# Optimization experiments

Measured on AMD Instinct MI355X. Metric: run time of the kernel, lower is better.

## Reference

```python
import jax, jax.numpy as jnp
import numpy as np

UP = 2
CUTOFF = 1.0 / UP  # factor = 1


def make_recon_rect(N, cutoff):
    """Reconstruction low-pass rect for rfft2, shape [N, N//2+1]."""
    lo = int(N * cutoff // 2)
    hi = int(N - lo)
    r = np.ones(N, dtype=np.float32)
    r[lo + 1:hi] = 0.0
    if N % 4 == 0:
        r[lo] = 0.5
        r[hi] = 0.5
    rect2d = r[:, None] * r[None, :]          # [N, N]
    return jnp.asarray(rect2d[:, :N // 2 + 1])  # keep rfft half-spectrum


def setup_inputs() -> dict:
    key = jax.random.key(0)
    x = jax.random.normal(key, (16, 64, 128, 128), dtype=jnp.float32)
    return {"x": x}


def reference(x):
    B, C, H, W = x.shape
    Hu, Wu = H * UP, W * UP
    # zero-insertion upsample: sample at (i*UP, j*UP), zeros elsewhere
    z = jnp.zeros((B, C, Hu, Wu), dtype=x.dtype).at[:, :, ::UP, ::UP].set(x)
    rect = make_recon_rect(Wu, CUTOFF)         # [Wu, Wu//2+1]
    xf = jnp.fft.rfft2(z) * rect               # low-pass in frequency domain
    out = jnp.fft.irfft2(xf) * (UP ** 2)       # gain correction
    return out
```

## Files before the change

kernel.cpp:

```cpp
#include <hip/hip_runtime.h>


typedef __bf16 bf16x8 __attribute__((ext_vector_type(8)));
typedef float  f32x4  __attribute__((ext_vector_type(4)));

#define W2 136
#define PI_F 3.14159265358979323846f

__device__ __forceinline__ unsigned short f2bf(float x) {
    unsigned int b = __float_as_uint(x);
    return (unsigned short)((b + 0x7FFFu + ((b >> 16) & 1u)) >> 16);
}

__device__ __forceinline__ float gfun(int j) {
    int d = 2 * (j & 127) + 1;
    float th = PI_F * (float)d * (1.0f / 256.0f);
    float s  = ((d & 3) == 1) ? 1.0f : -1.0f;
    return s * cosf(th) / (128.0f * sinf(th));
}

__global__ __launch_bounds__(512)
void init_ghtab(unsigned short* __restrict__ ghtab)
{
    const int t   = threadIdx.x;
    const int lane = t & 63;
    const int l15 = lane & 15;
    const int l4  = lane >> 4;
    const int dd  = t >> 6;
    const int base = l15 - 8 * l4 + 16 * dd;
    unsigned short u[8];
    #pragma unroll
    for (int e = 0; e < 8; ++e) u[e] = f2bf(gfun(base - e));
    ushort4 a = make_ushort4(u[0], u[1], u[2], u[3]);
    ushort4 b = make_ushort4(u[4], u[5], u[6], u[7]);
    *(ushort4*)&ghtab[t * 8]     = a;
    *(ushort4*)&ghtab[t * 8 + 4] = b;
}

__global__ __launch_bounds__(512, 4)
void upsample_fused(const float* __restrict__ xin, float* __restrict__ out,
                    const unsigned short* __restrict__ ghtab)
{
    __shared__ __align__(16) unsigned short Et[256 * W2];
    __shared__ float gtab[128];

    const int tid  = threadIdx.x;
    const int lane = tid & 63;
    const int w    = tid >> 6;
    const int l15  = lane & 15;
    const int l4   = lane >> 4;

    const float* __restrict__ xim = xin + (long long)blockIdx.x * (128 * 128);
    float*       __restrict__ oim = out + (long long)blockIdx.x * (256 * 256);

    const int r = 16 * w + l15;
    const float* __restrict__ xrow = xim + r * 128;

    float4 xlo[4], xhi[4];
    #pragma unroll
    for (int t = 0; t < 4; ++t) {
        xlo[t] = *(const float4*)&xrow[32 * t + 8 * l4];
        xhi[t] = *(const float4*)&xrow[32 * t + 8 * l4 + 4];
    }

    bf16x8 gh[8];
    if (ghtab) {
        #pragma unroll
        for (int dd = 0; dd < 8; ++dd)
            gh[dd] = *(const bf16x8*)&ghtab[(dd * 64 + lane) * 8];
    } else {
        if (tid < 128) gtab[tid] = gfun(tid);
        __syncthreads();
        #pragma unroll
        for (int dd = 0; dd < 8; ++dd) {
            union { bf16x8 v; unsigned short u[8]; } H;
            int base = l15 - 8 * l4 + 16 * dd;
            #pragma unroll
            for (int e = 0; e < 8; ++e) H.u[e] = f2bf(gtab[(base - e) & 127]);
            gh[dd] = H.v;
        }
    }

    bf16x8 xa[4];
    #pragma unroll
    for (int t = 0; t < 4; ++t) {
        union { bf16x8 v; unsigned short u[8]; } H;
        H.u[0] = f2bf(xlo[t].x); H.u[1] = f2bf(xlo[t].y);
        H.u[2] = f2bf(xlo[t].z); H.u[3] = f2bf(xlo[t].w);
        H.u[4] = f2bf(xhi[t].x); H.u[5] = f2bf(xhi[t].y);
        H.u[6] = f2bf(xhi[t].z); H.u[7] = f2bf(xhi[t].w);
        xa[t] = H.v;
        const int m0 = 32 * t + 8 * l4;
        #pragma unroll
        for (int e = 0; e < 8; ++e)
            Et[(2 * (m0 + e)) * W2 + r] = H.u[e];
    }

    float* __restrict__ orow = oim + (2 * r) * 256;
    #pragma unroll
    for (int mt = 0; mt < 8; ++mt) {
        f32x4 acc = {0.f, 0.f, 0.f, 0.f};
        #pragma unroll
        for (int t = 0; t < 4; ++t)
            acc = __builtin_amdgcn_mfma_f32_16x16x32_bf16(gh[(mt - 2 * t) & 7], xa[t], acc, 0, 0, 0);
        const int i0 = 16 * mt + 4 * l4;
        float4 xc = *(const float4*)&xrow[i0];
        float4 o0 = make_float4(xc.x, acc[0], xc.y, acc[1]);
        float4 o1 = make_float4(xc.z, acc[2], xc.w, acc[3]);
        *(float4*)&orow[2 * i0]     = o0;
        *(float4*)&orow[2 * i0 + 4] = o1;
        #pragma unroll
        for (int q = 0; q < 4; ++q)
            Et[(2 * (i0 + q) + 1) * W2 + r] = f2bf(acc[q]);
    }
    __syncthreads();

    {
        float* __restrict__ prow = oim + (2 * (16 * w + l15) + 1) * 256;
        #pragma unroll
        for (int mc = 0; mc < 16; ++mc) {
            f32x4 acc = {0.f, 0.f, 0.f, 0.f};
            #pragma unroll
            for (int t = 0; t < 4; ++t) {
                bf16x8 ef = *(const bf16x8*)&Et[(16 * mc + l15) * W2 + 32 * t + 8 * l4];
                acc = __builtin_amdgcn_mfma_f32_16x16x32_bf16(ef, gh[(w - 2 * t) & 7], acc, 0, 0, 0);
            }
            float4 o = make_float4(acc[0], acc[1], acc[2], acc[3]);
            *(float4*)&prow[16 * mc + 4 * l4] = o;
        }
    }
}

extern "C" void kernel_launch(void* const* d_in, const int* in_sizes, int n_in,
                              void* d_out, int out_size, void* d_ws, size_t ws_size,
                              hipStream_t stream)
{
    (void)n_in; (void)out_size;
    const float* x = (const float*)d_in[0];
    float* out = (float*)d_out;
    int nimg = in_sizes[0] / (128 * 128);

    unsigned short* ghtab = nullptr;
    if (ws_size >= 8192) {
        ghtab = (unsigned short*)d_ws;
        hipLaunchKernelGGL(init_ghtab, dim3(1), dim3(512), 0, stream, ghtab);
    }
    hipLaunchKernelGGL(upsample_fused, dim3(nimg), dim3(512), 0, stream, x, out, ghtab);
}
```

Before: 105.9 us.

## Split each image across two blocks by output column half, halving LDS

Each image is now handled by two blocks, each computing one half of the output columns. The split halves the shared-memory transpose buffer and raises the occupancy hint from 4 to 8 blocks per CU. Each block still loads the full input image and builds the full coefficient table, so that work is duplicated across the pair. Conversions now use native __bf16 casts instead of the manual rounding helper.

```diff
diff --git a/kernel.cpp b/kernel.cpp
--- a/kernel.cpp
+++ b/kernel.cpp
@@ -22,26 +22,24 @@
 __global__ __launch_bounds__(512)
 void init_ghtab(unsigned short* __restrict__ ghtab)
 {
-    const int t   = threadIdx.x;
+    const int t    = threadIdx.x;
     const int lane = t & 63;
-    const int l15 = lane & 15;
-    const int l4  = lane >> 4;
-    const int dd  = t >> 6;
+    const int l15  = lane & 15;
+    const int l4   = lane >> 4;
+    const int dd   = t >> 6;
     const int base = l15 - 8 * l4 + 16 * dd;
     unsigned short u[8];
     #pragma unroll
     for (int e = 0; e < 8; ++e) u[e] = f2bf(gfun(base - e));
-    ushort4 a = make_ushort4(u[0], u[1], u[2], u[3]);
-    ushort4 b = make_ushort4(u[4], u[5], u[6], u[7]);
-    *(ushort4*)&ghtab[t * 8]     = a;
-    *(ushort4*)&ghtab[t * 8 + 4] = b;
+    *(ushort4*)&ghtab[t * 8]     = make_ushort4(u[0], u[1], u[2], u[3]);
+    *(ushort4*)&ghtab[t * 8 + 4] = make_ushort4(u[4], u[5], u[6], u[7]);
 }
 
-__global__ __launch_bounds__(512, 4)
+__global__ __launch_bounds__(512, 8)
 void upsample_fused(const float* __restrict__ xin, float* __restrict__ out,
                     const unsigned short* __restrict__ ghtab)
 {
-    __shared__ __align__(16) unsigned short Et[256 * W2];
+    __shared__ __align__(16) __bf16 Et[128 * W2];
     __shared__ float gtab[128];
 
     const int tid  = threadIdx.x;
@@ -50,8 +48,10 @@
     const int l15  = lane & 15;
     const int l4   = lane >> 4;
 
-    const float* __restrict__ xim = xin + (long long)blockIdx.x * (128 * 128);
-    float*       __restrict__ oim = out + (long long)blockIdx.x * (256 * 256);
+    const long long img = blockIdx.x >> 1;
+    const int cb        = blockIdx.x & 1;
+    const float* __restrict__ xim = xin + img * (128LL * 128LL);
+    float*       __restrict__ oim = out + img * (256LL * 256LL);
 
     const int r = 16 * w + l15;
     const float* __restrict__ xrow = xim + r * 128;
@@ -81,49 +81,52 @@
         }
     }
 
-    bf16x8 xa[4];
+    union { bf16x8 v; __bf16 h[8]; } xa[4];
     #pragma unroll
     for (int t = 0; t < 4; ++t) {
-        union { bf16x8 v; unsigned short u[8]; } H;
-        H.u[0] = f2bf(xlo[t].x); H.u[1] = f2bf(xlo[t].y);
-        H.u[2] = f2bf(xlo[t].z); H.u[3] = f2bf(xlo[t].w);
-        H.u[4] = f2bf(xhi[t].x); H.u[5] = f2bf(xhi[t].y);
-        H.u[6] = f2bf(xhi[t].z); H.u[7] = f2bf(xhi[t].w);
-        xa[t] = H.v;
-        const int m0 = 32 * t + 8 * l4;
+        xa[t].h[0] = (__bf16)xlo[t].x; xa[t].h[1] = (__bf16)xlo[t].y;
+        xa[t].h[2] = (__bf16)xlo[t].z; xa[t].h[3] = (__bf16)xlo[t].w;
+        xa[t].h[4] = (__bf16)xhi[t].x; xa[t].h[5] = (__bf16)xhi[t].y;
+        xa[t].h[6] = (__bf16)xhi[t].z; xa[t].h[7] = (__bf16)xhi[t].w;
+    }
+    #pragma unroll
+    for (int tt = 0; tt < 2; ++tt) {
+        const int t = 2 * cb + tt;
         #pragma unroll
         for (int e = 0; e < 8; ++e)
-            Et[(2 * (m0 + e)) * W2 + r] = H.u[e];
+            Et[(64 * tt + 16 * l4 + 2 * e) * W2 + r] = xa[t].h[e];
     }
 
-    float* __restrict__ orow = oim + (2 * r) * 256;
+    float* __restrict__ orow = oim + (2 * r) * 256 + 128 * cb;
     #pragma unroll
-    for (int mt = 0; mt < 8; ++mt) {
+    for (int mt = 0; mt < 4; ++mt) {
         f32x4 acc = {0.f, 0.f, 0.f, 0.f};
         #pragma unroll
         for (int t = 0; t < 4; ++t)
-            acc = __builtin_amdgcn_mfma_f32_16x16x32_bf16(gh[(mt - 2 * t) & 7], xa[t], acc, 0, 0, 0);
-        const int i0 = 16 * mt + 4 * l4;
-        float4 xc = *(const float4*)&xrow[i0];
+            acc = __builtin_amdgcn_mfma_f32_16x16x32_bf16(gh[(4 * cb + mt - 2 * t) & 7],
+                                                          xa[t].v, acc, 0, 0, 0);
+        const int i0l = 16 * mt + 4 * l4;
+        float4 xc = *(const float4*)&xrow[64 * cb + i0l];
         float4 o0 = make_float4(xc.x, acc[0], xc.y, acc[1]);
         float4 o1 = make_float4(xc.z, acc[2], xc.w, acc[3]);
-        *(float4*)&orow[2 * i0]     = o0;
-        *(float4*)&orow[2 * i0 + 4] = o1;
+        *(float4*)&orow[2 * i0l]     = o0;
+        *(float4*)&orow[2 * i0l + 4] = o1;
         #pragma unroll
         for (int q = 0; q < 4; ++q)
-            Et[(2 * (i0 + q) + 1) * W2 + r] = f2bf(acc[q]);
+            Et[(2 * (i0l + q) + 1) * W2 + r] = (__bf16)acc[q];
     }
     __syncthreads();
 
     {
-        float* __restrict__ prow = oim + (2 * (16 * w + l15) + 1) * 256;
+        float* __restrict__ prow = oim + (2 * (16 * w + l15) + 1) * 256 + 128 * cb;
         #pragma unroll
-        for (int mc = 0; mc < 16; ++mc) {
+        for (int mc = 0; mc < 8; ++mc) {
             f32x4 acc = {0.f, 0.f, 0.f, 0.f};
             #pragma unroll
             for (int t = 0; t < 4; ++t) {
                 bf16x8 ef = *(const bf16x8*)&Et[(16 * mc + l15) * W2 + 32 * t + 8 * l4];
-                acc = __builtin_amdgcn_mfma_f32_16x16x32_bf16(ef, gh[(w - 2 * t) & 7], acc, 0, 0, 0);
+                acc = __builtin_amdgcn_mfma_f32_16x16x32_bf16(ef, gh[(w - 2 * t) & 7],
+                                                              acc, 0, 0, 0);
             }
             float4 o = make_float4(acc[0], acc[1], acc[2], acc[3]);
             *(float4*)&prow[16 * mc + 4 * l4] = o;
@@ -145,5 +148,5 @@
         ghtab = (unsigned short*)d_ws;
         hipLaunchKernelGGL(init_ghtab, dim3(1), dim3(512), 0, stream, ghtab);
     }
-    hipLaunchKernelGGL(upsample_fused, dim3(nimg), dim3(512), 0, stream, x, out, ghtab);
+    hipLaunchKernelGGL(upsample_fused, dim3(nimg * 2), dim3(512), 0, stream, x, out, ghtab);
 }
```

Result: slower. 194.7 us (+83.8%).
